# Kernel optimization log

Measured on AMD Instinct MI355X. Metric: run time of the kernel, lower is better.

The kernel has to match this reference:

```python
import jax, jax.numpy as jnp
import numpy as np

B, H, L, DK, DV = 8, 8, 1024, 64, 64
N = B * H
TEMP = 8.0  # sqrt(d_k)
A_MIX, B_MIX, C_MIX = 0.1, 0.4, 0.1


def setup_inputs() -> dict:
    key = jax.random.key(0)
    ks = jax.random.split(key, 6)
    q = jax.random.normal(ks[0], (N, L, DK), jnp.float32)
    k = jax.random.normal(ks[1], (N, L, DK), jnp.float32)
    v = jax.random.normal(ks[2], (N, L, DV), jnp.float32)
    q_rm = jax.random.normal(ks[3], (N, L, DK), jnp.float32)
    attn_pre = jax.random.normal(ks[4], (N, L, L), jnp.float32)
    conv_w = jax.random.normal(ks[5], (H, H, 3, 3), jnp.float32) * 0.05  # OIHW, no bias
    # causal mask: True where masked (j > i), broadcast over N
    mask = jnp.broadcast_to(jnp.triu(jnp.ones((L, L), bool), 1), (N, L, L))
    return {"q": q, "k": k, "v": v, "q_rm": q_rm, "attn_pre": attn_pre,
            "conv_w": conv_w, "mask": mask, "fg": 1}


def sift_down_right(src, filled):
    # R[..,1:,1:] = src[..,:-1,:-1]; R[..,0,:] = filled[..,0,:]; R[..,:,0] = filled[..,:,0]
    top = filled[:, 0:1, :]                    # [N,1,L]
    left = filled[:, 1:, 0:1]                  # [N,L-1,1]
    body = jnp.concatenate([left, src[:, :-1, :-1]], axis=-1)  # [N,L-1,L]
    return jnp.concatenate([top, body], axis=1)


def sift_down(src, filled):
    top = filled[:, 0:1, :]
    return jnp.concatenate([top, src[:, :-1, :]], axis=1)


def reference(q, k, v, q_rm, attn_pre, conv_w, mask, fg):
    attn = jnp.einsum('nqd,nkd->nqk', q, k) / TEMP
    attn_rm = jnp.einsum('nqd,nkd->nqk', q_rm, k) / TEMP
    # conv refinement of masked attn_rm, per (batch, head) grid
    x = jnp.where(mask, 0.0, attn_rm).reshape(-1, H, L, L)  # [B,H,L,L]
    x = jax.lax.conv_general_dilated(x, conv_w, (1, 1), 'SAME',
                                     dimension_numbers=('NCHW', 'OIHW', 'NCHW'))
    x = jax.nn.relu(x).reshape(-1, L, L)
    attn_cnn = sift_down_right(x, attn_rm) if fg == 1 else sift_down(x, attn_rm)
    attn_cnn = attn_cnn * C_MIX + attn_rm * (1.0 - C_MIX)
    attn = attn_cnn * B_MIX + attn * (1.0 - B_MIX)
    attn = attn_pre * A_MIX + attn * (1.0 - A_MIX)
    attn = jnp.where(mask, -jnp.inf, attn)
    attn = jax.nn.softmax(attn, axis=-1)
    # dropout is identity in eval/deterministic baseline
    out = jnp.einsum('nqk,nkd->nqd', attn, v)
    return out, attn
```

## Files before the change

kernel.cpp:

```cpp
#include <hip/hip_runtime.h>
#include <cstdint>
#include <cstddef>
#include <math.h>

#define L_ 1024
#define DK_ 64
#define DV_ 64
#define N_ 64
#define H_ 8
#define B_ 8

__device__ __forceinline__ float bcast(float v, int src) {
  return __int_as_float(__builtin_amdgcn_readlane(__float_as_int(v), src));
}

__global__ __launch_bounds__(256) void k1_qk_tril(
    const float* __restrict__ qrm, const float* __restrict__ kk,
    float* __restrict__ xm) {
  const int n  = blockIdx.z;
  const int q0 = blockIdx.y * 64;
  const int j0 = blockIdx.x * 64;
  const int t  = threadIdx.x;

  if (j0 > q0) {
    const float4 z = make_float4(0.f, 0.f, 0.f, 0.f);
    #pragma unroll
    for (int i = 0; i < 4; ++i) {
      const int row = (t >> 4) + i * 16;
      const int c4  = t & 15;
      float4* p = (float4*)(xm + ((size_t)(n * L_ + q0 + row)) * L_ + j0);
      p[c4] = z;
    }
    return;
  }

  __shared__ float As[64][65];
  __shared__ float Bs[64][65];
  #pragma unroll
  for (int i = 0; i < 4; ++i) {
    const int row = (t >> 4) + i * 16;
    const int c4  = t & 15;
    const float4 a = ((const float4*)(qrm + ((size_t)(n * L_ + q0 + row)) * DK_))[c4];
    const float4 b = ((const float4*)(kk  + ((size_t)(n * L_ + j0 + row)) * DK_))[c4];
    As[row][c4 * 4 + 0] = a.x; As[row][c4 * 4 + 1] = a.y;
    As[row][c4 * 4 + 2] = a.z; As[row][c4 * 4 + 3] = a.w;
    Bs[row][c4 * 4 + 0] = b.x; Bs[row][c4 * 4 + 1] = b.y;
    Bs[row][c4 * 4 + 2] = b.z; Bs[row][c4 * 4 + 3] = b.w;
  }
  __syncthreads();

  const int ty = t >> 4, tx = t & 15;
  float acc[4][4];
  #pragma unroll
  for (int i = 0; i < 4; ++i)
    #pragma unroll
    for (int j = 0; j < 4; ++j) acc[i][j] = 0.f;

  for (int d = 0; d < 64; ++d) {
    float a[4], b[4];
    #pragma unroll
    for (int i = 0; i < 4; ++i) a[i] = As[ty * 4 + i][d];
    #pragma unroll
    for (int j = 0; j < 4; ++j) b[j] = Bs[tx * 4 + j][d];
    #pragma unroll
    for (int i = 0; i < 4; ++i)
      #pragma unroll
      for (int j = 0; j < 4; ++j) acc[i][j] += a[i] * b[j];
  }

  #pragma unroll
  for (int i = 0; i < 4; ++i) {
    const int gq = q0 + ty * 4 + i;
    float* rowp = xm + ((size_t)(n * L_ + gq)) * L_;
    #pragma unroll
    for (int j = 0; j < 4; ++j) {
      const int gj = j0 + tx * 4 + j;
      rowp[gj] = (gj <= gq) ? acc[i][j] * 0.125f : 0.f;
    }
  }
}

__global__ __launch_bounds__(256) void k2_conv(
    const float* __restrict__ xm, const float* __restrict__ w,
    float* __restrict__ xs) {
  const int ct = blockIdx.x, rt = blockIdx.y, b = blockIdx.z;
  const int r0 = rt * 4, c0 = ct * 64;
  if (c0 > r0 + 4) return;

  __shared__ float in_s[8][6][68];
  __shared__ float ws[576];
  const int t = threadIdx.x;

  for (int i = t; i < 576; i += 256) ws[i] = w[i];
  for (int e = t; e < 8 * 6 * 66; e += 256) {
    const int hi  = e / 396;
    const int rem = e - hi * 396;
    const int rr  = rem / 66;
    const int cc  = rem - rr * 66;
    const int gr  = r0 - 1 + rr;
    const int gc  = c0 - 1 + cc;
    float v = 0.f;
    if (gr >= 0 && gr < L_ && gc >= 0 && gc < L_)
      v = xm[((size_t)((b * 8 + hi) * L_ + gr)) * L_ + gc];
    in_s[hi][rr][cc] = v;
  }
  __syncthreads();

  const int cc = t & 63;
  const int rr = t >> 6;
  float acc[8];
  #pragma unroll
  for (int ho = 0; ho < 8; ++ho) acc[ho] = 0.f;

  #pragma unroll
  for (int hi = 0; hi < 8; ++hi) {
    float iv[3][3];
    #pragma unroll
    for (int di = 0; di < 3; ++di)
      #pragma unroll
      for (int dj = 0; dj < 3; ++dj)
        iv[di][dj] = in_s[hi][rr + di][cc + dj];
    #pragma unroll
    for (int ho = 0; ho < 8; ++ho) {
      const float* wp = &ws[(ho * 8 + hi) * 9];
      #pragma unroll
      for (int di = 0; di < 3; ++di)
        #pragma unroll
        for (int dj = 0; dj < 3; ++dj)
          acc[ho] += iv[di][dj] * wp[di * 3 + dj];
    }
  }

  const int gr = r0 + rr, gc = c0 + cc;
  #pragma unroll
  for (int ho = 0; ho < 8; ++ho)
    xs[((size_t)((b * 8 + ho) * L_ + gr)) * L_ + gc] = fmaxf(acc[ho], 0.f);
}

__global__ __launch_bounds__(256) void k3_fused(
    const float* __restrict__ q, const float* __restrict__ kk,
    const float* __restrict__ v, const float* __restrict__ pre,
    const int* __restrict__ fgp, const float* __restrict__ xs,
    float* attn, float* __restrict__ out) {
  const int bid  = blockIdx.y * gridDim.x + blockIdx.x;
  const int work = (bid & 7) * 512 + (bid >> 3);
  const int n    = work >> 6;
  const int q0   = (63 - (work & 63)) * 16;

  const int t    = threadIdx.x;
  const int lane = t & 63;
  const int g    = t >> 6;
  const int fg   = *fgp;

  const int srow = t >> 4;
  const int c4   = t & 15;

  __shared__ float tb[2][64][65];

  const float* qb = q + ((size_t)(n * L_ + q0)) * DK_;
  float qreg[4];
  #pragma unroll
  for (int i = 0; i < 4; ++i) qreg[i] = qb[(size_t)(g + i * 4) * DK_ + lane];

  float m[4], l[4];
  #pragma unroll
  for (int i = 0; i < 4; ++i) { m[i] = -INFINITY; l[i] = 0.f; }

  int r_[4];
  #pragma unroll
  for (int i = 0; i < 4; ++i) r_[i] = q0 + g + i * 4;

  const int ntiles = (q0 >> 6) + 1;
  const float* kbase = kk + (size_t)n * L_ * DK_;

  #pragma unroll
  for (int i = 0; i < 4; ++i) {
    const int row = srow + i * 16;
    const float4 kx = *(const float4*)(kbase + (size_t)row * DK_ + c4 * 4);
    tb[0][c4 * 4 + 0][row] = kx.x;
    tb[0][c4 * 4 + 1][row] = kx.y;
    tb[0][c4 * 4 + 2][row] = kx.z;
    tb[0][c4 * 4 + 3][row] = kx.w;
  }
  __syncthreads();

  for (int tile = 0; tile < ntiles; ++tile) {
    const int cur = tile & 1, nxt = cur ^ 1;
    const int j0 = tile * 64;
    const int j  = j0 + lane;
    const bool havenext = (tile + 1) < ntiles;

    float4 kpre[4];
    if (havenext) {
      const float* kb2 = kbase + (size_t)(j0 + 64) * DK_;
      #pragma unroll
      for (int i = 0; i < 4; ++i)
        kpre[i] = *(const float4*)(kb2 + (size_t)(srow + i * 16) * DK_ + c4 * 4);
    }

    float rmv[4], prv[4], xsv[4];
    #pragma unroll
    for (int i = 0; i < 4; ++i) {
      const int r = r_[i];
      const bool act = (j <= r);
      rmv[i] = act ? attn[((size_t)(n * L_ + r)) * L_ + j] : 0.f;
      prv[i] = act ? pre[((size_t)(n * L_ + r)) * L_ + j] : 0.f;
      if (fg == 1)
        xsv[i] = (act && r > 0 && j > 0)
                     ? xs[((size_t)(n * L_ + r - 1)) * L_ + (j - 1)] : 0.f;
      else
        xsv[i] = (act && r > 0)
                     ? xs[((size_t)(n * L_ + r - 1)) * L_ + j] : 0.f;
    }

    float dot[4] = {0.f, 0.f, 0.f, 0.f};
    #pragma unroll
    for (int d = 0; d < 64; ++d) {
      const float kd = tb[cur][d][lane];
      #pragma unroll
      for (int i = 0; i < 4; ++i) dot[i] += bcast(qreg[i], d) * kd;
    }

    #pragma unroll
    for (int i = 0; i < 4; ++i) {
      const int r = r_[i];
      float s = -INFINITY;
      if (j <= r) {
        const float sqk = dot[i] * 0.125f;
        const float cnn = (fg == 1)
                              ? ((r == 0 || j == 0) ? rmv[i] : xsv[i])
                              : ((r == 0) ? rmv[i] : xsv[i]);
        const float mixed = cnn * 0.1f + rmv[i] * 0.9f;
        const float a2    = mixed * 0.4f + sqk * 0.6f;
        s = prv[i] * 0.1f + a2 * 0.9f;
      }
      attn[((size_t)(n * L_ + r)) * L_ + j] = s;

      float mt = s;
      #pragma unroll
      for (int o = 32; o > 0; o >>= 1) mt = fmaxf(mt, __shfl_xor(mt, o));
      const float mn = fmaxf(m[i], mt);
      float es = __expf(s - mn);
      #pragma unroll
      for (int o = 32; o > 0; o >>= 1) es += __shfl_xor(es, o);
      l[i] = l[i] * __expf(m[i] - mn) + es;
      m[i] = mn;
    }

    if (havenext) {
      #pragma unroll
      for (int i = 0; i < 4; ++i) {
        const int row = srow + i * 16;
        tb[nxt][c4 * 4 + 0][row] = kpre[i].x;
        tb[nxt][c4 * 4 + 1][row] = kpre[i].y;
        tb[nxt][c4 * 4 + 2][row] = kpre[i].z;
        tb[nxt][c4 * 4 + 3][row] = kpre[i].w;
      }
    }
    __syncthreads();
  }

  float invl[4];
  #pragma unroll
  for (int i = 0; i < 4; ++i) invl[i] = 1.f / l[i];

  float acc[4] = {0.f, 0.f, 0.f, 0.f};
  const float* vb = v + (size_t)n * L_ * DV_;

  #pragma unroll
  for (int i = 0; i < 4; ++i) {
    const int row = srow + i * 16;
    const float4 vx = *(const float4*)(vb + (size_t)row * DV_ + c4 * 4);
    tb[0][row][c4 * 4 + 0] = vx.x;
    tb[0][row][c4 * 4 + 1] = vx.y;
    tb[0][row][c4 * 4 + 2] = vx.z;
    tb[0][row][c4 * 4 + 3] = vx.w;
  }
  float s_cur[4];
  #pragma unroll
  for (int i = 0; i < 4; ++i)
    s_cur[i] = attn[((size_t)(n * L_ + r_[i])) * L_ + lane];
  __syncthreads();

  for (int tile = 0; tile < ntiles; ++tile) {
    const int cur = tile & 1, nxt = cur ^ 1;
    const int j0 = tile * 64;
    const int j  = j0 + lane;
    const bool havenext = (tile + 1) < ntiles;

    float4 vpre[4];
    float s_nxt[4];
    if (havenext) {
      const float* vb2 = vb + (size_t)(j0 + 64) * DV_;
      #pragma unroll
      for (int i = 0; i < 4; ++i)
        vpre[i] = *(const float4*)(vb2 + (size_t)(srow + i * 16) * DV_ + c4 * 4);
      #pragma unroll
      for (int i = 0; i < 4; ++i)
        s_nxt[i] = attn[((size_t)(n * L_ + r_[i])) * L_ + j + 64];
    }

    float p[4];
    #pragma unroll
    for (int i = 0; i < 4; ++i) {
      p[i] = __expf(s_cur[i] - m[i]) * invl[i];
      attn[((size_t)(n * L_ + r_[i])) * L_ + j] = p[i];
    }

    #pragma unroll
    for (int c = 0; c < 64; ++c) {
      const float vv = tb[cur][c][lane];
      #pragma unroll
      for (int i = 0; i < 4; ++i) acc[i] += bcast(p[i], c) * vv;
    }

    if (havenext) {
      #pragma unroll
      for (int i = 0; i < 4; ++i) {
        const int row = srow + i * 16;
        tb[nxt][row][c4 * 4 + 0] = vpre[i].x;
        tb[nxt][row][c4 * 4 + 1] = vpre[i].y;
        tb[nxt][row][c4 * 4 + 2] = vpre[i].z;
        tb[nxt][row][c4 * 4 + 3] = vpre[i].w;
      }
      #pragma unroll
      for (int i = 0; i < 4; ++i) s_cur[i] = s_nxt[i];
    }
    __syncthreads();
  }

  #pragma unroll
  for (int i = 0; i < 4; ++i)
    out[((size_t)(n * L_ + r_[i])) * DV_ + lane] = acc[i];
}

extern "C" void kernel_launch(void* const* d_in, const int* in_sizes, int n_in,
                              void* d_out, int out_size, void* d_ws,
                              size_t ws_size, hipStream_t stream) {
  const float* q   = (const float*)d_in[0];
  const float* kk  = (const float*)d_in[1];
  const float* v   = (const float*)d_in[2];
  const float* qrm = (const float*)d_in[3];
  const float* pre = (const float*)d_in[4];
  const float* cw  = (const float*)d_in[5];
  const int* fg = (const int*)d_in[7];

  float* out  = (float*)d_out;
  float* attn = out + (size_t)N_ * L_ * DV_;
  float* xs   = (float*)d_ws;

  k1_qk_tril<<<dim3(16, 16, 64), 256, 0, stream>>>(qrm, kk, attn);
  k2_conv<<<dim3(16, 256, 8), 256, 0, stream>>>(attn, cw, xs);
  k3_fused<<<dim3(64, 64), 256, 0, stream>>>(q, kk, v, pre, fg, xs, attn, out);
}
```

Before: 1.620 ms.

## Stage Q and P rows in LDS with swizzled K tiles, defer softmax reductions

Replaces the per-element readlane broadcasts of Q and P in the QK and PV inner loops with float4 LDS reads from a shared Q/P buffer. K tiles are stored row-major with an XOR swizzle instead of a padded transpose. The per-tile cross-lane max and sum reductions for the online softmax become per-lane running stats that are merged once after the loop. P is computed one tile ahead and double-buffered in LDS, which adds LDS traffic and some extra bookkeeping.

New measurement: 1.474 ms. 9.0% less time.

```diff
diff --git a/kernel.cpp b/kernel.cpp
--- a/kernel.cpp
+++ b/kernel.cpp
@@ -9,10 +9,6 @@
 #define N_ 64
 #define H_ 8
 #define B_ 8
-
-__device__ __forceinline__ float bcast(float v, int src) {
-  return __int_as_float(__builtin_amdgcn_readlane(__float_as_int(v), src));
-}
 
 __global__ __launch_bounds__(256) void k1_qk_tril(
     const float* __restrict__ qrm, const float* __restrict__ kk,
@@ -155,34 +151,37 @@
   const int srow = t >> 4;
   const int c4   = t & 15;
 
-  __shared__ float tb[2][64][65];
-
-  const float* qb = q + ((size_t)(n * L_ + q0)) * DK_;
-  float qreg[4];
-  #pragma unroll
-  for (int i = 0; i < 4; ++i) qreg[i] = qb[(size_t)(g + i * 4) * DK_ + lane];
-
-  float m[4], l[4];
-  #pragma unroll
-  for (int i = 0; i < 4; ++i) { m[i] = -INFINITY; l[i] = 0.f; }
-
-  int r_[4];
-  #pragma unroll
-  for (int i = 0; i < 4; ++i) r_[i] = q0 + g + i * 4;
+  __shared__ float tiles[2][64][64];
+  __shared__ float qps[2][16][64];
+
+  int r_[4], lr_[4];
+  #pragma unroll
+  for (int i = 0; i < 4; ++i) { r_[i] = q0 + g + i * 4; lr_[i] = g + i * 4; }
+  size_t rowoff[4];
+  #pragma unroll
+  for (int i = 0; i < 4; ++i) rowoff[i] = ((size_t)(n * L_ + r_[i])) * L_;
 
   const int ntiles = (q0 >> 6) + 1;
   const float* kbase = kk + (size_t)n * L_ * DK_;
-
+  const int wswz = (c4 ^ srow) << 2;
+  const int lx = lane & 15;
+
+  {
+    const float4 qx =
+        *(const float4*)(q + ((size_t)(n * L_ + q0 + srow)) * DK_ + c4 * 4);
+    *(float4*)&qps[0][srow][c4 * 4] = qx;
+  }
   #pragma unroll
   for (int i = 0; i < 4; ++i) {
     const int row = srow + i * 16;
     const float4 kx = *(const float4*)(kbase + (size_t)row * DK_ + c4 * 4);
-    tb[0][c4 * 4 + 0][row] = kx.x;
-    tb[0][c4 * 4 + 1][row] = kx.y;
-    tb[0][c4 * 4 + 2][row] = kx.z;
-    tb[0][c4 * 4 + 3][row] = kx.w;
+    *(float4*)&tiles[0][row][wswz] = kx;
   }
   __syncthreads();
+
+  float m[4], l[4];
+  #pragma unroll
+  for (int i = 0; i < 4; ++i) { m[i] = -1e30f; l[i] = 0.f; }
 
   for (int tile = 0; tile < ntiles; ++tile) {
     const int cur = tile & 1, nxt = cur ^ 1;
@@ -203,22 +202,25 @@
     for (int i = 0; i < 4; ++i) {
       const int r = r_[i];
       const bool act = (j <= r);
-      rmv[i] = act ? attn[((size_t)(n * L_ + r)) * L_ + j] : 0.f;
-      prv[i] = act ? pre[((size_t)(n * L_ + r)) * L_ + j] : 0.f;
+      rmv[i] = act ? attn[rowoff[i] + j] : 0.f;
+      prv[i] = act ? pre[rowoff[i] + j] : 0.f;
       if (fg == 1)
         xsv[i] = (act && r > 0 && j > 0)
-                     ? xs[((size_t)(n * L_ + r - 1)) * L_ + (j - 1)] : 0.f;
+                     ? xs[rowoff[i] - L_ + (j - 1)] : 0.f;
       else
-        xsv[i] = (act && r > 0)
-                     ? xs[((size_t)(n * L_ + r - 1)) * L_ + j] : 0.f;
+        xsv[i] = (act && r > 0) ? xs[rowoff[i] - L_ + j] : 0.f;
     }
 
     float dot[4] = {0.f, 0.f, 0.f, 0.f};
-    #pragma unroll
-    for (int d = 0; d < 64; ++d) {
-      const float kd = tb[cur][d][lane];
-      #pragma unroll
-      for (int i = 0; i < 4; ++i) dot[i] += bcast(qreg[i], d) * kd;
+    const float* krow = &tiles[cur][0][0] + lane * 64;
+    #pragma unroll 4
+    for (int gg = 0; gg < 16; ++gg) {
+      const float4 kq = *(const float4*)(krow + ((gg ^ lx) << 2));
+      #pragma unroll
+      for (int i = 0; i < 4; ++i) {
+        const float4 q4 = *(const float4*)&qps[0][lr_[i]][gg << 2];
+        dot[i] += q4.x * kq.x + q4.y * kq.y + q4.z * kq.z + q4.w * kq.w;
+      }
     }
 
     #pragma unroll
@@ -234,16 +236,10 @@
         const float a2    = mixed * 0.4f + sqk * 0.6f;
         s = prv[i] * 0.1f + a2 * 0.9f;
       }
-      attn[((size_t)(n * L_ + r)) * L_ + j] = s;
-
-      float mt = s;
-      #pragma unroll
-      for (int o = 32; o > 0; o >>= 1) mt = fmaxf(mt, __shfl_xor(mt, o));
-      const float mn = fmaxf(m[i], mt);
-      float es = __expf(s - mn);
-      #pragma unroll
-      for (int o = 32; o > 0; o >>= 1) es += __shfl_xor(es, o);
-      l[i] = l[i] * __expf(m[i] - mn) + es;
+      attn[rowoff[i] + j] = s;
+
+      const float mn = fmaxf(m[i], s);
+      l[i] = l[i] * __expf(m[i] - mn) + __expf(s - mn);
       m[i] = mn;
     }
 
@@ -251,13 +247,22 @@
       #pragma unroll
       for (int i = 0; i < 4; ++i) {
         const int row = srow + i * 16;
-        tb[nxt][c4 * 4 + 0][row] = kpre[i].x;
-        tb[nxt][c4 * 4 + 1][row] = kpre[i].y;
-        tb[nxt][c4 * 4 + 2][row] = kpre[i].z;
-        tb[nxt][c4 * 4 + 3][row] = kpre[i].w;
+        *(float4*)&tiles[nxt][row][wswz] = kpre[i];
       }
     }
     __syncthreads();
+  }
+
+  #pragma unroll
+  for (int i = 0; i < 4; ++i) {
+    float mf = m[i];
+    #pragma unroll
+    for (int o = 32; o > 0; o >>= 1) mf = fmaxf(mf, __shfl_xor(mf, o));
+    float ls = l[i] * __expf(m[i] - mf);
+    #pragma unroll
+    for (int o = 32; o > 0; o >>= 1) ls += __shfl_xor(ls, o);
+    m[i] = mf;
+    l[i] = ls;
   }
 
   float invl[4];
@@ -271,21 +276,20 @@
   for (int i = 0; i < 4; ++i) {
     const int row = srow + i * 16;
     const float4 vx = *(const float4*)(vb + (size_t)row * DV_ + c4 * 4);
-    tb[0][row][c4 * 4 + 0] = vx.x;
-    tb[0][row][c4 * 4 + 1] = vx.y;
-    tb[0][row][c4 * 4 + 2] = vx.z;
-    tb[0][row][c4 * 4 + 3] = vx.w;
-  }
-  float s_cur[4];
-  #pragma unroll
-  for (int i = 0; i < 4; ++i)
-    s_cur[i] = attn[((size_t)(n * L_ + r_[i])) * L_ + lane];
+    *(float4*)&tiles[0][row][c4 * 4] = vx;
+  }
+  #pragma unroll
+  for (int i = 0; i < 4; ++i) {
+    const float s  = attn[rowoff[i] + lane];
+    const float pv = __expf(s - m[i]) * invl[i];
+    qps[0][lr_[i]][lane] = pv;
+    attn[rowoff[i] + lane] = pv;
+  }
   __syncthreads();
 
   for (int tile = 0; tile < ntiles; ++tile) {
     const int cur = tile & 1, nxt = cur ^ 1;
     const int j0 = tile * 64;
-    const int j  = j0 + lane;
     const bool havenext = (tile + 1) < ntiles;
 
     float4 vpre[4];
@@ -297,34 +301,35 @@
         vpre[i] = *(const float4*)(vb2 + (size_t)(srow + i * 16) * DV_ + c4 * 4);
       #pragma unroll
       for (int i = 0; i < 4; ++i)
-        s_nxt[i] = attn[((size_t)(n * L_ + r_[i])) * L_ + j + 64];
-    }
-
-    float p[4];
-    #pragma unroll
-    for (int i = 0; i < 4; ++i) {
-      p[i] = __expf(s_cur[i] - m[i]) * invl[i];
-      attn[((size_t)(n * L_ + r_[i])) * L_ + j] = p[i];
-    }
-
-    #pragma unroll
-    for (int c = 0; c < 64; ++c) {
-      const float vv = tb[cur][c][lane];
-      #pragma unroll
-      for (int i = 0; i < 4; ++i) acc[i] += bcast(p[i], c) * vv;
+        s_nxt[i] = attn[rowoff[i] + j0 + 64 + lane];
+    }
+
+    #pragma unroll 4
+    for (int cs = 0; cs < 16; ++cs) {
+      const int c0 = cs * 4;
+      const float v0 = tiles[cur][c0 + 0][lane];
+      const float v1 = tiles[cur][c0 + 1][lane];
+      const float v2 = tiles[cur][c0 + 2][lane];
+      const float v3 = tiles[cur][c0 + 3][lane];
+      #pragma unroll
+      for (int i = 0; i < 4; ++i) {
+        const float4 pr = *(const float4*)&qps[cur][lr_[i]][c0];
+        acc[i] += pr.x * v0 + pr.y * v1 + pr.z * v2 + pr.w * v3;
+      }
     }
 
     if (havenext) {
       #pragma unroll
       for (int i = 0; i < 4; ++i) {
         const int row = srow + i * 16;
-        tb[nxt][row][c4 * 4 + 0] = vpre[i].x;
-        tb[nxt][row][c4 * 4 + 1] = vpre[i].y;
-        tb[nxt][row][c4 * 4 + 2] = vpre[i].z;
-        tb[nxt][row][c4 * 4 + 3] = vpre[i].w;
-      }
-      #pragma unroll
-      for (int i = 0; i < 4; ++i) s_cur[i] = s_nxt[i];
+        *(float4*)&tiles[nxt][row][c4 * 4] = vpre[i];
+      }
+      #pragma unroll
+      for (int i = 0; i < 4; ++i) {
+        const float pv = __expf(s_nxt[i] - m[i]) * invl[i];
+        qps[nxt][lr_[i]][lane] = pv;
+        attn[rowoff[i] + j0 + 64 + lane] = pv;
+      }
     }
     __syncthreads();
   }
```
